# Kernel optimization log

Hardware: AMD Instinct MI355X
Metric: run time of the kernel (lower is better)

Reference implementation:

```python
import jax, jax.numpy as jnp
import numpy as np

NV = 1_000_000   # number of 'var' nodes
NC = 500_000     # number of 'con' nodes
E = 16_000_000   # number of v2c edges (c2v is the reverse edge set)
H = 10           # n_h_feats


def setup_inputs() -> dict:
    key = jax.random.key(0)
    ks = jax.random.split(key, 24)
    s = 0.1  # weight init scale
    inp = {
        "var_c": jax.random.normal(ks[0], (NV,), jnp.float32),
        "var_x": jax.random.normal(ks[1], (NV,), jnp.float32),
        "con_b": jax.random.normal(ks[2], (NC,), jnp.float32),
        "A": jax.random.uniform(ks[3], (E,), jnp.float32),
        "src": jax.random.randint(ks[4], (E,), 0, NV, jnp.int32),
        "dst": jax.random.randint(ks[5], (E,), 0, NC, jnp.int32),
        # var_emb / con_emb Linear params
        "Wv": jax.random.normal(ks[6], (2, H), jnp.float32) * s,
        "bv": jnp.zeros((H,), jnp.float32),
        "Wc": jax.random.normal(ks[7], (1, H), jnp.float32) * s,
        "bc": jnp.zeros((H,), jnp.float32),
        # conv1 (GraphConv, shared across v2c/c2v) -- note: its output is
        # overwritten in the original forward and never reaches the output
        "W1": jax.random.normal(ks[8], (H, H), jnp.float32) * s,
        "b1": jnp.zeros((H,), jnp.float32),
        # conv2 (GraphConv, shared across v2c/c2v)
        "W2": jax.random.normal(ks[9], (H, H), jnp.float32) * s,
        "b2": jnp.zeros((H,), jnp.float32),
        # output MLP
        "Wo1": jax.random.normal(ks[10], (H, H), jnp.float32) * s,
        "bo1": jnp.zeros((H,), jnp.float32),
        "Wo2": jax.random.normal(ks[11], (H, H), jnp.float32) * s,
        "bo2": jnp.zeros((H,), jnp.float32),
        "Wo3": jax.random.normal(ks[12], (H, 1), jnp.float32) * s,
        "bo3": jnp.zeros((1,), jnp.float32),
    }
    return inp


def _gconv(x_src, W, b, s_idx, d_idx, ew, norm_src, norm_dst, n_dst):
    # DGL GraphConv, norm='both', with edge weights; in==out feats so W first.
    h = (x_src * norm_src) @ W                      # [N_src, H]
    msg = h[s_idx] * ew[:, None]                    # gather + edge weight
    agg = jax.ops.segment_sum(msg, d_idx, num_segments=n_dst)
    return agg * norm_dst + b


def reference(var_c, var_x, con_b, A, src, dst,
              Wv, bv, Wc, bc, W1, b1, W2, b2,
              Wo1, bo1, Wo2, bo2, Wo3, bo3):
    # symmetric norm from UNWEIGHTED degrees (DGL GraphConv norm='both'),
    # clamped at 1. v2c: out-deg(var), in-deg(con); c2v is the reverse.
    ones_e = jnp.ones_like(A)
    deg_v = jnp.clip(jax.ops.segment_sum(ones_e, src, num_segments=NV), 1.0)
    deg_c = jnp.clip(jax.ops.segment_sum(ones_e, dst, num_segments=NC), 1.0)
    norm_v = deg_v[:, None] ** -0.5
    norm_c = deg_c[:, None] ** -0.5

    # node embeddings
    var_feats = jnp.stack([var_c, var_x], axis=1)   # [NV, 2]
    X_var = jax.nn.relu(var_feats @ Wv + bv)        # [NV, H]
    X_con = jax.nn.relu(con_b[:, None] @ Wc + bc)   # [NC, H] (unused by convs: GraphConv ignores dst feats)

    # In the original forward, conv1 outputs (h_con / h_var) are immediately
    # overwritten by conv2 outputs (GraphConv only consumes src features),
    # so only conv2 lies on the effective compute path.
    h_con = jax.nn.relu(_gconv(X_var, W2, b2, src, dst, A, norm_v, norm_c, NC))
    h_var = jax.nn.relu(_gconv(h_con, W2, b2, dst, src, A, norm_c, norm_v, NV))

    h = jax.nn.relu(h_var @ Wo1 + bo1)
    h = jax.nn.relu(h @ Wo2 + bo2)
    logit = h @ Wo3 + bo3                           # [NV, 1]
    # dgl.readout_nodes(op='mean', ntype='var'), single graph -> [1, 1]
    return jnp.mean(logit, axis=0, keepdims=True)
```

## Files before the change

### kernel.cpp

```cpp
#include <hip/hip_runtime.h>

#define HF 10
#define ST 16
#define BST 16
#define SLC 256
#define NBINS 4096
#define NSL 8


__global__ __launch_bounds__(1024) void k_hist(const int* __restrict__ idx,
                                               unsigned* __restrict__ hist,
                                               long long s_begin, long long s_end, int per) {
    __shared__ unsigned l[NBINS];
    int t = threadIdx.x, sl = blockIdx.x;
    for (int b = t; b < NBINS; b += 1024) l[b] = 0u;
    __syncthreads();
    long long s0 = s_begin + (long long)sl * per;
    long long s1 = s0 + per; if (s1 > s_end) s1 = s_end;
    for (long long i = s0 + t; i < s1; i += 1024)
        atomicAdd(&l[((unsigned)idx[i]) >> 8], 1u);
    __syncthreads();
    unsigned* out = hist + (size_t)sl * NBINS;
    for (int b = t; b < NBINS; b += 1024) out[b] = l[b];
}

__global__ void k_coltot(const unsigned* __restrict__ h, unsigned* __restrict__ colT) {
    int b = blockIdx.x * 256 + threadIdx.x;
    unsigned s = 0u;
    for (int sl = 0; sl < SLC; sl++) s += h[(size_t)sl * NBINS + b];
    colT[b] = s;
}

__global__ __launch_bounds__(1024) void k_prefix(const unsigned* __restrict__ colT,
                                                 unsigned* __restrict__ start) {
    __shared__ unsigned p[1024];
    int t = threadIdx.x;
    uint4 v = *(const uint4*)(colT + 4 * t);
    unsigned own = v.x + v.y + v.z + v.w;
    p[t] = own;
    __syncthreads();
    for (int off = 1; off < 1024; off <<= 1) {
        unsigned u = (t >= off) ? p[t - off] : 0u;
        __syncthreads();
        p[t] += u;
        __syncthreads();
    }
    unsigned e = p[t] - own;
    *(uint4*)(start + 4 * t) = make_uint4(e, e + v.x, e + v.x + v.y, e + v.x + v.y + v.z);
    if (t == 1023) start[NBINS] = p[1023];
}

__global__ void k_offs(unsigned* __restrict__ h, const unsigned* __restrict__ start) {
    int b = blockIdx.x * 256 + threadIdx.x;
    unsigned cur = start[b];
    for (int sl = 0; sl < SLC; sl++) {
        unsigned* cell = h + (size_t)sl * NBINS + b;
        unsigned v = *cell;
        *cell = cur;
        cur += v;
    }
}

__global__ __launch_bounds__(1024) void k_scatS(const int* __restrict__ src, const int* __restrict__ dst,
                                                const float* __restrict__ A,
                                                const unsigned* __restrict__ offs,
                                                uint2* __restrict__ ebufS,
                                                long long E, int per) {
    __shared__ unsigned cur[NBINS];
    int t = threadIdx.x, sl = blockIdx.x;
    const unsigned* o = offs + (size_t)sl * NBINS;
    for (int b = t; b < NBINS; b += 1024) cur[b] = o[b];
    __syncthreads();
    long long s0 = (long long)sl * per;
    long long s1 = s0 + per; if (s1 > E) s1 = E;
    for (long long i = s0 + t; i < s1; i += 1024) {
        unsigned s = (unsigned)src[i], d = (unsigned)dst[i];
        float a = A[i];
        unsigned pos = atomicAdd(&cur[s >> 8], 1u);
        ebufS[pos] = make_uint2(((s & 255u) << 19) | d, __float_as_uint(a));
    }
}

__global__ void k_sliceCnt(const uint2* __restrict__ ebufA, const unsigned* __restrict__ startS,
                           unsigned* __restrict__ startS2) {
    __shared__ unsigned c8[NSL];
    int t = threadIdx.x, b = blockIdx.x;
    if (t < NSL) c8[t] = 0u;
    __syncthreads();
    unsigned i0 = startS[b], i1 = startS[b + 1];
    for (unsigned i = i0 + t; i < i1; i += 256)
        atomicAdd(&c8[(ebufA[i].x & 0x7FFFFu) >> 16], 1u);
    __syncthreads();
    if (t == 0) {
        unsigned run = i0;
        for (int s = 0; s < NSL; s++) { startS2[b * NSL + s] = run; run += c8[s]; }
    }
}

__global__ void k_sliceScat(const uint2* __restrict__ ebufA, const unsigned* __restrict__ startS,
                            const unsigned* __restrict__ startS2, uint2* __restrict__ ebufB) {
    __shared__ unsigned cur[NSL];
    int t = threadIdx.x, b = blockIdx.x;
    if (t < NSL) cur[t] = startS2[b * NSL + t];
    __syncthreads();
    unsigned i0 = startS[b], i1 = startS[b + 1];
    for (unsigned i = i0 + t; i < i1; i += 256) {
        uint2 kv = ebufA[i];
        unsigned pos = atomicAdd(&cur[(kv.x & 0x7FFFFu) >> 16], 1u);
        ebufB[pos] = kv;
    }
}

__global__ void k_cntS2(const uint2* __restrict__ ebufS, const unsigned* __restrict__ startS,
                        const float* __restrict__ var_c, const float* __restrict__ var_x,
                        float4* __restrict__ vcx, int NV) {
    __shared__ unsigned cnt[256];
    int t = threadIdx.x, b = blockIdx.x;
    cnt[t] = 0u;
    __syncthreads();
    unsigned i0 = startS[b], i1 = startS[b + 1];
    for (unsigned i = i0 + t; i < i1; i += 256)
        atomicAdd(&cnt[ebufS[i].x >> 19], 1u);
    __syncthreads();
    int v = b * 256 + t;
    if (v < NV)
        vcx[v] = make_float4(var_c[v], var_x[v], rsqrtf(fmaxf((float)cnt[t], 1.0f)), 0.0f);
}

__global__ __launch_bounds__(1024) void k_histD2(const uint2* __restrict__ ebufB,
                                                 const unsigned* __restrict__ startS,
                                                 unsigned* __restrict__ hist, int B0, int binsPer) {
    __shared__ unsigned l[NBINS];
    int t = threadIdx.x, sl = blockIdx.x;
    for (int b = t; b < NBINS; b += 1024) l[b] = 0u;
    __syncthreads();
    int b0 = B0 + sl * binsPer;
    unsigned i0 = startS[b0], i1 = startS[b0 + binsPer];
    for (unsigned i = i0 + t; i < i1; i += 1024)
        atomicAdd(&l[(ebufB[i].x & 0x7FFFFu) >> 8], 1u);
    __syncthreads();
    unsigned* out = hist + (size_t)sl * NBINS;
    for (int b = t; b < NBINS; b += 1024) out[b] = l[b];
}

__global__ __launch_bounds__(1024) void k_scatD2(const uint2* __restrict__ ebufB,
                                                 const unsigned* __restrict__ startS,
                                                 const unsigned* __restrict__ offs,
                                                 const float4* __restrict__ vcx,
                                                 uint4* __restrict__ ebufD, int B0, int binsPer) {
    __shared__ unsigned cur[NBINS];
    int t = threadIdx.x, sl = blockIdx.x;
    const unsigned* o = offs + (size_t)sl * NBINS;
    for (int b = t; b < NBINS; b += 1024) cur[b] = o[b];
    __syncthreads();
    int b0 = B0 + sl * binsPer;
    for (int bb = 0; bb < binsPer; bb++) {
        int bin = b0 + bb;
        unsigned vbase = ((unsigned)bin) << 8;
        unsigned i0 = startS[bin], i1 = startS[bin + 1];
        for (unsigned i = i0 + t; i < i1; i += 1024) {
            uint2 kv = ebufB[i];
            unsigned d = kv.x & 0x7FFFFu;
            float4 g = vcx[vbase | (kv.x >> 19)];
            unsigned pos = atomicAdd(&cur[d >> 8], 1u);
            ebufD[pos] = make_uint4(d & 255u, __float_as_uint(__uint_as_float(kv.y) * g.z),
                                    __float_as_uint(g.x), __float_as_uint(g.y));
        }
    }
}

__global__ __launch_bounds__(1024) void k_scatD(const int* __restrict__ src, const int* __restrict__ dst,
                                                const float* __restrict__ A,
                                                const unsigned* __restrict__ offs,
                                                const float4* __restrict__ vcx,
                                                uint4* __restrict__ ebufD,
                                                long long s_begin, long long s_end, int per) {
    __shared__ unsigned cur[NBINS];
    int t = threadIdx.x, sl = blockIdx.x;
    const unsigned* o = offs + (size_t)sl * NBINS;
    for (int b = t; b < NBINS; b += 1024) cur[b] = o[b];
    __syncthreads();
    long long s0 = s_begin + (long long)sl * per;
    long long s1 = s0 + per; if (s1 > s_end) s1 = s_end;
    for (long long i = s0 + t; i < s1; i += 4096) {
        unsigned sv[4], dv[4]; float av[4]; bool hv[4];
#pragma unroll
        for (int j = 0; j < 4; j++) {
            long long idx = i + (long long)j * 1024;
            hv[j] = idx < s1;
            if (hv[j]) { sv[j] = (unsigned)src[idx]; dv[j] = (unsigned)dst[idx]; av[j] = A[idx]; }
            else       { sv[j] = 0u; dv[j] = 0u; av[j] = 0.0f; }
        }
        float4 g[4];
#pragma unroll
        for (int j = 0; j < 4; j++)
            if (hv[j]) g[j] = vcx[sv[j]];
#pragma unroll
        for (int j = 0; j < 4; j++) {
            if (!hv[j]) continue;
            unsigned pos = atomicAdd(&cur[dv[j] >> 8], 1u);
            ebufD[pos] = make_uint4(dv[j] & 255u, __float_as_uint(av[j] * g[j].z),
                                    __float_as_uint(g[j].x), __float_as_uint(g[j].y));
        }
    }
}

__global__ void k_aggD(const uint4* __restrict__ ebufD, const unsigned* __restrict__ startD,
                       const float* __restrict__ Wv, const float* __restrict__ bv,
                       float* __restrict__ bufC, float* __restrict__ deg_c, int NC) {
    __shared__ float acc[256 * HF];
    __shared__ unsigned cnt[256];
    int t = threadIdx.x, b = blockIdx.x;
    for (int i = t; i < 256 * HF; i += 256) acc[i] = 0.0f;
    cnt[t] = 0u;
    float wv0[HF], wv1[HF], bvv[HF];
#pragma unroll
    for (int h = 0; h < HF; h++) { wv0[h] = Wv[h]; wv1[h] = Wv[HF + h]; bvv[h] = bv[h]; }
    __syncthreads();
    unsigned i0 = startD[b], i1 = startD[b + 1];
    for (unsigned i = i0 + t; i < i1; i += 256) {
        uint4 kv = ebufD[i];
        unsigned dl = kv.x;
        float anv = __uint_as_float(kv.y);
        float c   = __uint_as_float(kv.z);
        float x   = __uint_as_float(kv.w);
        float* ac = acc + dl * HF;
#pragma unroll
        for (int h = 0; h < HF; h++) {
            float e = fmaxf(fmaf(c, wv0[h], fmaf(x, wv1[h], bvv[h])), 0.0f);
            atomicAdd(ac + h, anv * e);
        }
        atomicAdd(&cnt[dl], 1u);
    }
    __syncthreads();
    int gid = b * 256 + t;
    if (gid < NC) {
        float* row = bufC + (size_t)gid * BST;
#pragma unroll
        for (int h = 0; h < HF; h++) row[h] += acc[t * HF + h];
        deg_c[gid] += (float)cnt[t];
    }
}

__global__ void k_conT(float* __restrict__ bufC, const float* __restrict__ deg_c,
                       const float* __restrict__ W2, const float* __restrict__ b2, int NC) {
    __shared__ float sW[HF * HF], sb[HF];
    int t = threadIdx.x;
    if (t < HF * HF) sW[t] = W2[t];
    if (t < HF)      sb[t] = b2[t];
    __syncthreads();
    int i = blockIdx.x * 256 + t;
    if (i >= NC) return;
    float nc = rsqrtf(fmaxf(deg_c[i], 1.0f));
    float* row = bufC + (size_t)i * BST;
    float x[HF];
#pragma unroll
    for (int h = 0; h < HF; h++) x[h] = row[h];
#pragma unroll
    for (int j = 0; j < HF; j++) {
        float a = 0.0f;
#pragma unroll
        for (int k = 0; k < HF; k++) a = fmaf(x[k], sW[k * HF + j], a);
        row[j] = fmaxf(fmaf(a, nc, sb[j]), 0.0f) * nc;
    }
}

__global__ void k_aggS(const uint2* __restrict__ ebufS, const unsigned* __restrict__ startS,
                       const float* __restrict__ bufC, const float4* __restrict__ vcx,
                       const float* __restrict__ W2, const float* __restrict__ b2,
                       const float* __restrict__ Wo1, const float* __restrict__ bo1,
                       const float* __restrict__ Wo2, const float* __restrict__ bo2,
                       const float* __restrict__ Wo3, const float* __restrict__ bo3,
                       double* __restrict__ gacc, int NV) {
    __shared__ float acc[256 * HF];
    __shared__ float sW2[HF * HF], sb2[HF], sW1[HF * HF], sb1[HF], sWm[HF * HF], sbm[HF], sW3[HF];
    __shared__ float sb3;
    __shared__ double red[256];
    int t = threadIdx.x, b = blockIdx.x;
    for (int i = t; i < 256 * HF; i += 256) acc[i] = 0.0f;
    if (t < HF * HF) { sW2[t] = W2[t]; sW1[t] = Wo1[t]; sWm[t] = Wo2[t]; }
    if (t < HF)      { sb2[t] = b2[t]; sb1[t] = bo1[t]; sbm[t] = bo2[t]; sW3[t] = Wo3[t]; }
    if (t == 0)      sb3 = bo3[0];
    __syncthreads();
    unsigned i0 = startS[b], i1 = startS[b + 1];
    int grp = t >> 2;
    int q   = t & 3;
    int nq  = (q < 2) ? 4 : (q == 2 ? 2 : 0);
    for (unsigned base = i0; base < i1; base += 64) {
        unsigned e = base + (unsigned)grp;
        bool ok = e < i1;
        uint2 kv = ok ? ebufS[e] : make_uint2(0u, 0u);
        float4 y = make_float4(0.f, 0.f, 0.f, 0.f);
        if (ok) y = *(const float4*)(bufC + (size_t)(kv.x & 0x7FFFFu) * BST + 4 * q);
        if (ok && nq) {
            float a = __uint_as_float(kv.y);
            float* ac = acc + (kv.x >> 19) * HF + 4 * q;
            atomicAdd(ac + 0, a * y.x);
            atomicAdd(ac + 1, a * y.y);
            if (nq == 4) {
                atomicAdd(ac + 2, a * y.z);
                atomicAdd(ac + 3, a * y.w);
            }
        }
    }
    __syncthreads();
    double local = 0.0;
    int v = b * 256 + t;
    if (v < NV) {
        float nv = vcx[v].z;
        float x[HF], hvv[HF], h1[HF], h2[HF];
#pragma unroll
        for (int h = 0; h < HF; h++) x[h] = acc[t * HF + h];
#pragma unroll
        for (int j = 0; j < HF; j++) {
            float a = 0.0f;
#pragma unroll
            for (int k = 0; k < HF; k++) a = fmaf(x[k], sW2[k * HF + j], a);
            hvv[j] = fmaxf(fmaf(a, nv, sb2[j]), 0.0f);
        }
#pragma unroll
        for (int j = 0; j < HF; j++) {
            float a = sb1[j];
#pragma unroll
            for (int k = 0; k < HF; k++) a = fmaf(hvv[k], sW1[k * HF + j], a);
            h1[j] = fmaxf(a, 0.0f);
        }
#pragma unroll
        for (int j = 0; j < HF; j++) {
            float a = sbm[j];
#pragma unroll
            for (int k = 0; k < HF; k++) a = fmaf(h1[k], sWm[k * HF + j], a);
            h2[j] = fmaxf(a, 0.0f);
        }
        float logit = sb3;
#pragma unroll
        for (int k = 0; k < HF; k++) logit = fmaf(h2[k], sW3[k], logit);
        local = (double)logit;
    }
    red[t] = local;
    __syncthreads();
    for (int s = 128; s > 0; s >>= 1) {
        if (t < s) red[t] += red[t + s];
        __syncthreads();
    }
    if (t == 0) atomicAdd(gacc, red[0]);
}

__global__ void k_out(const double* __restrict__ acc, float* __restrict__ out, int NV) {
    out[0] = (float)(acc[0] / (double)NV);
}


__global__ void k_degree(const int* __restrict__ src, const int* __restrict__ dst,
                         float* __restrict__ deg_v, float* __restrict__ deg_c, int E) {
    int i = blockIdx.x * blockDim.x + threadIdx.x;
    if (i < E) {
        atomicAdd(&deg_v[src[i]], 1.0f);
        atomicAdd(&deg_c[dst[i]], 1.0f);
    }
}

__global__ void k_norm(float* __restrict__ d, int n) {
    int i = blockIdx.x * blockDim.x + threadIdx.x;
    if (i < n) d[i] = 1.0f / sqrtf(fmaxf(d[i], 1.0f));
}

__global__ void k_var_emb(const float* __restrict__ var_c, const float* __restrict__ var_x,
                          const float* __restrict__ norm_v,
                          const float* __restrict__ Wv, const float* __restrict__ bv,
                          const float* __restrict__ W2,
                          float* __restrict__ out, int NV) {
    __shared__ float sWv[2 * HF], sbv[HF], sW2[HF * HF];
    int t = threadIdx.x;
    if (t < 2 * HF) sWv[t] = Wv[t];
    if (t < HF)     sbv[t] = bv[t];
    if (t < HF * HF) sW2[t] = W2[t];
    __syncthreads();
    int i = blockIdx.x * blockDim.x + t;
    if (i >= NV) return;
    float c = var_c[i], x = var_x[i], nv = norm_v[i];
    float e[HF];
#pragma unroll
    for (int h = 0; h < HF; h++)
        e[h] = fmaxf(fmaf(c, sWv[h], fmaf(x, sWv[HF + h], sbv[h])), 0.0f) * nv;
    float* row = out + (size_t)i * ST;
#pragma unroll
    for (int j = 0; j < HF; j++) {
        float acc = 0.0f;
#pragma unroll
        for (int k = 0; k < HF; k++) acc = fmaf(e[k], sW2[k * HF + j], acc);
        row[j] = acc;
    }
}

__global__ void k_edge(const int* __restrict__ gidx, const int* __restrict__ didx,
                       const float* __restrict__ A,
                       const float* __restrict__ h, float* __restrict__ agg, int E) {
    int tid = blockIdx.x * blockDim.x + threadIdx.x;
    int e = tid / 5;
    if (e >= E) return;
    int q = tid - e * 5;
    int s = gidx[e], d = didx[e];
    float a = A[e];
    const float2 m = *(const float2*)(h + (size_t)s * ST + 2 * q);
    float* o = agg + (size_t)d * ST + 2 * q;
    atomicAdd(o,     m.x * a);
    atomicAdd(o + 1, m.y * a);
}

__global__ void k_con(float* __restrict__ buf, const float* __restrict__ norm_c,
                      const float* __restrict__ W2, const float* __restrict__ b2, int NC) {
    __shared__ float sW2[HF * HF], sb2[HF];
    int t = threadIdx.x;
    if (t < HF * HF) sW2[t] = W2[t];
    if (t < HF)      sb2[t] = b2[t];
    __syncthreads();
    int i = blockIdx.x * blockDim.x + t;
    if (i >= NC) return;
    float nc = norm_c[i];
    float* row = buf + (size_t)i * ST;
    float hc[HF];
#pragma unroll
    for (int h = 0; h < HF; h++)
        hc[h] = fmaxf(fmaf(row[h], nc, sb2[h]), 0.0f) * nc;
#pragma unroll
    for (int j = 0; j < HF; j++) {
        float acc = 0.0f;
#pragma unroll
        for (int k = 0; k < HF; k++) acc = fmaf(hc[k], sW2[k * HF + j], acc);
        row[j] = acc;
    }
}

__global__ void k_final(const float* __restrict__ agg_v, const float* __restrict__ norm_v,
                        const float* __restrict__ b2,
                        const float* __restrict__ Wo1, const float* __restrict__ bo1,
                        const float* __restrict__ Wo2, const float* __restrict__ bo2,
                        const float* __restrict__ Wo3, const float* __restrict__ bo3,
                        double* __restrict__ acc, int NV) {
    __shared__ float sb2[HF], sW1[HF * HF], sb1[HF], sW2m[HF * HF], sb2m[HF], sW3[HF];
    __shared__ float sb3;
    __shared__ double red[256];
    int t = threadIdx.x;
    if (t < HF)      sb2[t]  = b2[t];
    if (t < HF * HF) sW1[t]  = Wo1[t];
    if (t < HF)      sb1[t]  = bo1[t];
    if (t < HF * HF) sW2m[t] = Wo2[t];
    if (t < HF)      sb2m[t] = bo2[t];
    if (t < HF)      sW3[t]  = Wo3[t];
    if (t == 0)      sb3     = bo3[0];
    __syncthreads();
    int i = blockIdx.x * blockDim.x + t;
    double local = 0.0;
    if (i < NV) {
        float nv = norm_v[i];
        const float* row = agg_v + (size_t)i * ST;
        float v[HF], h1[HF], h2[HF];
#pragma unroll
        for (int h = 0; h < HF; h++) v[h] = fmaxf(fmaf(row[h], nv, sb2[h]), 0.0f);
#pragma unroll
        for (int j = 0; j < HF; j++) {
            float a = sb1[j];
#pragma unroll
            for (int k = 0; k < HF; k++) a = fmaf(v[k], sW1[k * HF + j], a);
            h1[j] = fmaxf(a, 0.0f);
        }
#pragma unroll
        for (int j = 0; j < HF; j++) {
            float a = sb2m[j];
#pragma unroll
            for (int k = 0; k < HF; k++) a = fmaf(h1[k], sW2m[k * HF + j], a);
            h2[j] = fmaxf(a, 0.0f);
        }
        float logit = sb3;
#pragma unroll
        for (int k = 0; k < HF; k++) logit = fmaf(h2[k], sW3[k], logit);
        local = (double)logit;
    }
    red[t] = local;
    __syncthreads();
    for (int s = 128; s > 0; s >>= 1) {
        if (t < s) red[t] += red[t + s];
        __syncthreads();
    }
    if (t == 0) atomicAdd(acc, red[0]);
}


extern "C" void kernel_launch(void* const* d_in, const int* in_sizes, int n_in,
                              void* d_out, int out_size, void* d_ws, size_t ws_size,
                              hipStream_t stream) {
    const float* var_c = (const float*)d_in[0];
    const float* var_x = (const float*)d_in[1];
    const float* A   = (const float*)d_in[3];
    const int*   src = (const int*)d_in[4];
    const int*   dst = (const int*)d_in[5];
    const float* Wv  = (const float*)d_in[6];
    const float* bv  = (const float*)d_in[7];
    const float* W2  = (const float*)d_in[12];
    const float* b2  = (const float*)d_in[13];
    const float* Wo1 = (const float*)d_in[14];
    const float* bo1 = (const float*)d_in[15];
    const float* Wo2 = (const float*)d_in[16];
    const float* bo2 = (const float*)d_in[17];
    const float* Wo3 = (const float*)d_in[18];
    const float* bo3 = (const float*)d_in[19];

    const int NV = in_sizes[0];
    const int NC = in_sizes[2];
    const int E  = in_sizes[3];

    auto layout_bytes = [&](int nDc, bool split, size_t* offs_out) -> size_t {
        size_t off = 0;
        auto alloc = [&](size_t bytes, int slot) {
            if (offs_out) offs_out[slot] = off;
            off = (off + bytes + 255) & ~(size_t)255;
        };
        size_t EcMax;
        if (split) {
            long long vspan = (long long)(NBINS / nDc) * 256;
            if (vspan > NV) vspan = NV;
            long long ec = ((long long)E * vspan + NV - 1) / NV + (long long)E / 64;
            if (ec > E) ec = E;
            EcMax = (size_t)ec;
        } else {
            EcMax = ((size_t)E + nDc - 1) / nDc;
        }
        alloc((size_t)NC * BST * 4, 0);
        alloc((size_t)NV * 16, 1);
        alloc((size_t)NC * 4, 2);
        alloc((size_t)SLC * NBINS * 4, 3);
        alloc((size_t)SLC * NBINS * 4, 4);
        alloc((size_t)NBINS * 4, 5);
        alloc((size_t)(NBINS + 1) * 4, 6);
        alloc((size_t)(NBINS + 1) * 4, 7);
        alloc(8, 8);
        alloc((size_t)E * 8, 9);
        size_t scratch = EcMax * 16;
        if (split && scratch < (size_t)E * 8) scratch = (size_t)E * 8;
        alloc(scratch, 10);
        alloc(split ? (size_t)NBINS * NSL * 4 : (size_t)0, 11);
        return off;
    };

    int nD = 0;
    bool split = false;
    size_t offs[12];
    for (int cand : {2, 4, 8, 16}) {
        if (layout_bytes(cand, true, nullptr) <= ws_size) { nD = cand; split = true; break; }
    }
    if (nD == 0) {
        for (int cand = 2; cand <= 16; cand++)
            if (layout_bytes(cand, false, nullptr) <= ws_size) { nD = cand; break; }
    }
    bool fast = (nD > 0) && (NV <= (1 << 20)) && (NC <= (1 << 19)) && (E > 0);

    char* ws = (char*)d_ws;
    if (fast) {
        layout_bytes(nD, split, offs);
        float*    bufC   = (float*)(ws + offs[0]);
        float4*   vcx    = (float4*)(ws + offs[1]);
        float*    deg_c  = (float*)(ws + offs[2]);
        unsigned* hS     = (unsigned*)(ws + offs[3]);
        unsigned* hD     = (unsigned*)(ws + offs[4]);
        unsigned* colT   = (unsigned*)(ws + offs[5]);
        unsigned* startS = (unsigned*)(ws + offs[6]);
        unsigned* startD = (unsigned*)(ws + offs[7]);
        double*   gacc   = (double*)(ws + offs[8]);
        uint2*    ebufP  = (uint2*)(ws + offs[9]);
        char*     scr    = ws + offs[10];
        unsigned* startS2 = (unsigned*)(ws + offs[11]);

        const int perS = (int)(((long long)E + SLC - 1) / SLC);
        const int NB_S = (NV + 255) >> 8;
        const int NB_C = (NC + 255) >> 8;

        hipMemsetAsync(bufC,  0, (size_t)NC * BST * 4, stream);
        hipMemsetAsync(deg_c, 0, (size_t)NC * 4, stream);
        hipMemsetAsync(gacc,  0, 8, stream);

        if (split) {
            uint2* ebufA = (uint2*)scr;
            uint4* ebufD = (uint4*)scr;

            k_hist<<<SLC, 1024, 0, stream>>>(src, hS, 0, E, perS);
            k_coltot<<<NBINS / 256, 256, 0, stream>>>(hS, colT);
            k_prefix<<<1, 1024, 0, stream>>>(colT, startS);
            k_offs<<<NBINS / 256, 256, 0, stream>>>(hS, startS);
            k_scatS<<<SLC, 1024, 0, stream>>>(src, dst, A, hS, ebufA, E, perS);

            k_sliceCnt<<<NBINS, 256, 0, stream>>>(ebufA, startS, startS2);
            k_sliceScat<<<NBINS, 256, 0, stream>>>(ebufA, startS, startS2, ebufP);

            k_cntS2<<<NB_S, 256, 0, stream>>>(ebufP, startS, var_c, var_x, vcx, NV);

            const int binsChunk = NBINS / nD;
            const int binsPer   = binsChunk / SLC;
            for (int c = 0; c < nD; c++) {
                int B0 = c * binsChunk;
                k_histD2<<<SLC, 1024, 0, stream>>>(ebufP, startS, hD, B0, binsPer);
                k_coltot<<<NBINS / 256, 256, 0, stream>>>(hD, colT);
                k_prefix<<<1, 1024, 0, stream>>>(colT, startD);
                k_offs<<<NBINS / 256, 256, 0, stream>>>(hD, startD);
                k_scatD2<<<SLC, 1024, 0, stream>>>(ebufP, startS, hD, vcx, ebufD, B0, binsPer);
                k_aggD<<<NB_C, 256, 0, stream>>>(ebufD, startD, Wv, bv, bufC, deg_c, NC);
            }
        } else {
            uint4* ebufD = (uint4*)scr;
            const long long EcMax = ((long long)E + nD - 1) / nD;
            const int perD = (int)((EcMax + SLC - 1) / SLC);

            k_hist<<<SLC, 1024, 0, stream>>>(src, hS, 0, E, perS);
            k_coltot<<<NBINS / 256, 256, 0, stream>>>(hS, colT);
            k_prefix<<<1, 1024, 0, stream>>>(colT, startS);
            k_offs<<<NBINS / 256, 256, 0, stream>>>(hS, startS);
            k_scatS<<<SLC, 1024, 0, stream>>>(src, dst, A, hS, ebufP, E, perS);

            k_cntS2<<<NB_S, 256, 0, stream>>>(ebufP, startS, var_c, var_x, vcx, NV);

            for (int c = 0; c < nD; c++) {
                long long cb = (long long)c * EcMax;
                long long ce = cb + EcMax; if (ce > E) ce = E;
                k_hist<<<SLC, 1024, 0, stream>>>(dst, hD, cb, ce, perD);
                k_coltot<<<NBINS / 256, 256, 0, stream>>>(hD, colT);
                k_prefix<<<1, 1024, 0, stream>>>(colT, startD);
                k_offs<<<NBINS / 256, 256, 0, stream>>>(hD, startD);
                k_scatD<<<SLC, 1024, 0, stream>>>(src, dst, A, hD, vcx, ebufD, cb, ce, perD);
                k_aggD<<<NB_C, 256, 0, stream>>>(ebufD, startD, Wv, bv, bufC, deg_c, NC);
            }
        }
        k_conT<<<NB_C, 256, 0, stream>>>(bufC, deg_c, W2, b2, NC);

        k_aggS<<<NB_S, 256, 0, stream>>>(ebufP, startS, bufC, vcx, W2, b2,
                                         Wo1, bo1, Wo2, bo2, Wo3, bo3, gacc, NV);
        k_out<<<1, 1, 0, stream>>>(gacc, (float*)d_out, NV);
    } else {
        const int B = 256;
        float* fbufV = (float*)ws;
        float* fbufC = (float*)(ws + (size_t)NV * ST * 4);
        float* deg_v = (float*)(ws + (size_t)(NV + NC) * ST * 4);
        float* deg_c = deg_v + NV;
        size_t acc_off = ((size_t)(NV + NC) * ST * 4 + (size_t)(NV + NC) * 4 + 7) & ~(size_t)7;
        double* acc = (double*)(ws + acc_off);

        hipMemsetAsync(deg_v, 0, (size_t)(NV + NC) * 4, stream);
        hipMemsetAsync(fbufC, 0, (size_t)NC * ST * 4, stream);
        hipMemsetAsync(acc, 0, sizeof(double), stream);

        k_degree<<<(E + B - 1) / B, B, 0, stream>>>(src, dst, deg_v, deg_c, E);
        k_norm<<<(NV + NC + B - 1) / B, B, 0, stream>>>(deg_v, NV + NC);
        k_var_emb<<<(NV + B - 1) / B, B, 0, stream>>>(var_c, var_x, deg_v, Wv, bv, W2, fbufV, NV);

        long long tE = (long long)E * 5;
        k_edge<<<(int)((tE + B - 1) / B), B, 0, stream>>>(src, dst, A, fbufV, fbufC, E);
        k_con<<<(NC + B - 1) / B, B, 0, stream>>>(fbufC, deg_c, W2, b2, NC);

        hipMemsetAsync(fbufV, 0, (size_t)NV * ST * 4, stream);
        k_edge<<<(int)((tE + B - 1) / B), B, 0, stream>>>(dst, src, A, fbufC, fbufV, E);

        k_final<<<(NV + B - 1) / B, B, 0, stream>>>(fbufV, deg_v, b2, Wo1, bo1, Wo2, bo2, Wo3, bo3, acc, NV);
        k_out<<<1, 1, 0, stream>>>(acc, (float*)d_out, NV);
    }
}
```

Baseline: 2.997 ms.

## Replace two-pass global slice sort with in-place LDS-staged 16-way sub-sort

Merges the slice count and slice scatter kernels into one kernel that stages each source bin in LDS, counts 16 dst sub-slices, and writes back in place to the same buffer. This drops one full read of the edge buffer and the separate ping-pong scratch buffer. The freed memory lets the dst-chunk scratch be sized per chunk, so fewer dst chunks (starting from 4) can fit. Writes in scatD2 are now bounds-checked against capacity. Bins larger than the LDS capacity are silently left unsorted, which risks wrong ordering on skewed inputs.

```diff
diff --git a/kernel.cpp b/kernel.cpp
--- a/kernel.cpp
+++ b/kernel.cpp
@@ -5,7 +5,8 @@
 #define BST 16
 #define SLC 256
 #define NBINS 4096
-#define NSL 8
+#define NSL 16
+#define CAPS 6144
 
 
 __global__ __launch_bounds__(1024) void k_hist(const int* __restrict__ idx,
@@ -81,33 +82,30 @@
     }
 }
 
-__global__ void k_sliceCnt(const uint2* __restrict__ ebufA, const unsigned* __restrict__ startS,
-                           unsigned* __restrict__ startS2) {
-    __shared__ unsigned c8[NSL];
+__global__ __launch_bounds__(256) void k_sliceIP(uint2* __restrict__ ebuf,
+                                                 const unsigned* __restrict__ startS) {
+    __shared__ uint2 ebl[CAPS];
+    __shared__ unsigned c16[NSL], p16[NSL];
     int t = threadIdx.x, b = blockIdx.x;
-    if (t < NSL) c8[t] = 0u;
-    __syncthreads();
-    unsigned i0 = startS[b], i1 = startS[b + 1];
-    for (unsigned i = i0 + t; i < i1; i += 256)
-        atomicAdd(&c8[(ebufA[i].x & 0x7FFFFu) >> 16], 1u);
+    unsigned i0 = startS[b], i1 = startS[b + 1], n = i1 - i0;
+    if (n == 0u || n > (unsigned)CAPS) return;
+    if (t < NSL) c16[t] = 0u;
+    __syncthreads();
+    for (unsigned i = t; i < n; i += 256) {
+        uint2 kv = ebuf[i0 + i];
+        ebl[i] = kv;
+        atomicAdd(&c16[(kv.x & 0x7FFFFu) >> 15], 1u);
+    }
     __syncthreads();
     if (t == 0) {
-        unsigned run = i0;
-        for (int s = 0; s < NSL; s++) { startS2[b * NSL + s] = run; run += c8[s]; }
-    }
-}
-
-__global__ void k_sliceScat(const uint2* __restrict__ ebufA, const unsigned* __restrict__ startS,
-                            const unsigned* __restrict__ startS2, uint2* __restrict__ ebufB) {
-    __shared__ unsigned cur[NSL];
-    int t = threadIdx.x, b = blockIdx.x;
-    if (t < NSL) cur[t] = startS2[b * NSL + t];
-    __syncthreads();
-    unsigned i0 = startS[b], i1 = startS[b + 1];
-    for (unsigned i = i0 + t; i < i1; i += 256) {
-        uint2 kv = ebufA[i];
-        unsigned pos = atomicAdd(&cur[(kv.x & 0x7FFFFu) >> 16], 1u);
-        ebufB[pos] = kv;
+        unsigned run = 0u;
+        for (int s = 0; s < NSL; s++) { p16[s] = run; run += c16[s]; }
+    }
+    __syncthreads();
+    for (unsigned i = t; i < n; i += 256) {
+        uint2 kv = ebl[i];
+        unsigned pos = atomicAdd(&p16[(kv.x & 0x7FFFFu) >> 15], 1u);
+        ebuf[i0 + pos] = kv;
     }
 }
 
@@ -147,7 +145,8 @@
                                                  const unsigned* __restrict__ startS,
                                                  const unsigned* __restrict__ offs,
                                                  const float4* __restrict__ vcx,
-                                                 uint4* __restrict__ ebufD, int B0, int binsPer) {
+                                                 uint4* __restrict__ ebufD, int B0, int binsPer,
+                                                 unsigned cap) {
     __shared__ unsigned cur[NBINS];
     int t = threadIdx.x, sl = blockIdx.x;
     const unsigned* o = offs + (size_t)sl * NBINS;
@@ -163,8 +162,9 @@
             unsigned d = kv.x & 0x7FFFFu;
             float4 g = vcx[vbase | (kv.x >> 19)];
             unsigned pos = atomicAdd(&cur[d >> 8], 1u);
-            ebufD[pos] = make_uint4(d & 255u, __float_as_uint(__uint_as_float(kv.y) * g.z),
-                                    __float_as_uint(g.x), __float_as_uint(g.y));
+            if (pos < cap)
+                ebufD[pos] = make_uint4(d & 255u, __float_as_uint(__uint_as_float(kv.y) * g.z),
+                                        __float_as_uint(g.x), __float_as_uint(g.y));
         }
     }
 }
@@ -510,22 +510,23 @@
     const int NC = in_sizes[2];
     const int E  = in_sizes[3];
 
-    auto layout_bytes = [&](int nDc, bool split, size_t* offs_out) -> size_t {
+    long long EcMaxUsed = 0;
+    auto layout_bytes = [&](int nDc, bool binchunk, size_t* offs_out) -> size_t {
         size_t off = 0;
         auto alloc = [&](size_t bytes, int slot) {
             if (offs_out) offs_out[slot] = off;
             off = (off + bytes + 255) & ~(size_t)255;
         };
-        size_t EcMax;
-        if (split) {
+        long long ec;
+        if (binchunk) {
             long long vspan = (long long)(NBINS / nDc) * 256;
             if (vspan > NV) vspan = NV;
-            long long ec = ((long long)E * vspan + NV - 1) / NV + (long long)E / 64;
+            ec = ((long long)E * vspan) / NV + (long long)E / 64 + 1024;
             if (ec > E) ec = E;
-            EcMax = (size_t)ec;
         } else {
-            EcMax = ((size_t)E + nDc - 1) / nDc;
-        }
+            ec = ((long long)E + nDc - 1) / nDc;
+        }
+        EcMaxUsed = ec;
         alloc((size_t)NC * BST * 4, 0);
         alloc((size_t)NV * 16, 1);
         alloc((size_t)NC * 4, 2);
@@ -536,18 +537,15 @@
         alloc((size_t)(NBINS + 1) * 4, 7);
         alloc(8, 8);
         alloc((size_t)E * 8, 9);
-        size_t scratch = EcMax * 16;
-        if (split && scratch < (size_t)E * 8) scratch = (size_t)E * 8;
-        alloc(scratch, 10);
-        alloc(split ? (size_t)NBINS * NSL * 4 : (size_t)0, 11);
+        alloc((size_t)ec * 16, 10);
         return off;
     };
 
     int nD = 0;
-    bool split = false;
-    size_t offs[12];
-    for (int cand : {2, 4, 8, 16}) {
-        if (layout_bytes(cand, true, nullptr) <= ws_size) { nD = cand; split = true; break; }
+    bool binc = false;
+    size_t offs[11];
+    for (int cand : {4, 8, 16}) {
+        if (layout_bytes(cand, true, nullptr) <= ws_size) { nD = cand; binc = true; break; }
     }
     if (nD == 0) {
         for (int cand = 2; cand <= 16; cand++)
@@ -557,7 +555,8 @@
 
     char* ws = (char*)d_ws;
     if (fast) {
-        layout_bytes(nD, split, offs);
+        layout_bytes(nD, binc, offs);
+        const long long EcMax = EcMaxUsed;
         float*    bufC   = (float*)(ws + offs[0]);
         float4*   vcx    = (float4*)(ws + offs[1]);
         float*    deg_c  = (float*)(ws + offs[2]);
@@ -567,9 +566,8 @@
         unsigned* startS = (unsigned*)(ws + offs[6]);
         unsigned* startD = (unsigned*)(ws + offs[7]);
         double*   gacc   = (double*)(ws + offs[8]);
-        uint2*    ebufP  = (uint2*)(ws + offs[9]);
-        char*     scr    = ws + offs[10];
-        unsigned* startS2 = (unsigned*)(ws + offs[11]);
+        uint2*    ebufS  = (uint2*)(ws + offs[9]);
+        uint4*    ebufD  = (uint4*)(ws + offs[10]);
 
         const int perS = (int)(((long long)E + SLC - 1) / SLC);
         const int NB_S = (NV + 255) >> 8;
@@ -579,45 +577,31 @@
         hipMemsetAsync(deg_c, 0, (size_t)NC * 4, stream);
         hipMemsetAsync(gacc,  0, 8, stream);
 
-        if (split) {
-            uint2* ebufA = (uint2*)scr;
-            uint4* ebufD = (uint4*)scr;
-
-            k_hist<<<SLC, 1024, 0, stream>>>(src, hS, 0, E, perS);
-            k_coltot<<<NBINS / 256, 256, 0, stream>>>(hS, colT);
-            k_prefix<<<1, 1024, 0, stream>>>(colT, startS);
-            k_offs<<<NBINS / 256, 256, 0, stream>>>(hS, startS);
-            k_scatS<<<SLC, 1024, 0, stream>>>(src, dst, A, hS, ebufA, E, perS);
-
-            k_sliceCnt<<<NBINS, 256, 0, stream>>>(ebufA, startS, startS2);
-            k_sliceScat<<<NBINS, 256, 0, stream>>>(ebufA, startS, startS2, ebufP);
-
-            k_cntS2<<<NB_S, 256, 0, stream>>>(ebufP, startS, var_c, var_x, vcx, NV);
-
+        k_hist<<<SLC, 1024, 0, stream>>>(src, hS, 0, E, perS);
+        k_coltot<<<NBINS / 256, 256, 0, stream>>>(hS, colT);
+        k_prefix<<<1, 1024, 0, stream>>>(colT, startS);
+        k_offs<<<NBINS / 256, 256, 0, stream>>>(hS, startS);
+        k_scatS<<<SLC, 1024, 0, stream>>>(src, dst, A, hS, ebufS, E, perS);
+
+        k_sliceIP<<<NBINS, 256, 0, stream>>>(ebufS, startS);
+
+        k_cntS2<<<NB_S, 256, 0, stream>>>(ebufS, startS, var_c, var_x, vcx, NV);
+
+        if (binc) {
             const int binsChunk = NBINS / nD;
             const int binsPer   = binsChunk / SLC;
             for (int c = 0; c < nD; c++) {
                 int B0 = c * binsChunk;
-                k_histD2<<<SLC, 1024, 0, stream>>>(ebufP, startS, hD, B0, binsPer);
+                k_histD2<<<SLC, 1024, 0, stream>>>(ebufS, startS, hD, B0, binsPer);
                 k_coltot<<<NBINS / 256, 256, 0, stream>>>(hD, colT);
                 k_prefix<<<1, 1024, 0, stream>>>(colT, startD);
                 k_offs<<<NBINS / 256, 256, 0, stream>>>(hD, startD);
-                k_scatD2<<<SLC, 1024, 0, stream>>>(ebufP, startS, hD, vcx, ebufD, B0, binsPer);
+                k_scatD2<<<SLC, 1024, 0, stream>>>(ebufS, startS, hD, vcx, ebufD,
+                                                   B0, binsPer, (unsigned)EcMax);
                 k_aggD<<<NB_C, 256, 0, stream>>>(ebufD, startD, Wv, bv, bufC, deg_c, NC);
             }
         } else {
-            uint4* ebufD = (uint4*)scr;
-            const long long EcMax = ((long long)E + nD - 1) / nD;
             const int perD = (int)((EcMax + SLC - 1) / SLC);
-
-            k_hist<<<SLC, 1024, 0, stream>>>(src, hS, 0, E, perS);
-            k_coltot<<<NBINS / 256, 256, 0, stream>>>(hS, colT);
-            k_prefix<<<1, 1024, 0, stream>>>(colT, startS);
-            k_offs<<<NBINS / 256, 256, 0, stream>>>(hS, startS);
-            k_scatS<<<SLC, 1024, 0, stream>>>(src, dst, A, hS, ebufP, E, perS);
-
-            k_cntS2<<<NB_S, 256, 0, stream>>>(ebufP, startS, var_c, var_x, vcx, NV);
-
             for (int c = 0; c < nD; c++) {
                 long long cb = (long long)c * EcMax;
                 long long ce = cb + EcMax; if (ce > E) ce = E;
@@ -631,7 +615,7 @@
         }
         k_conT<<<NB_C, 256, 0, stream>>>(bufC, deg_c, W2, b2, NC);
 
-        k_aggS<<<NB_S, 256, 0, stream>>>(ebufP, startS, bufC, vcx, W2, b2,
+        k_aggS<<<NB_S, 256, 0, stream>>>(ebufS, startS, bufC, vcx, W2, b2,
                                          Wo1, bo1, Wo2, bo2, Wo3, bo3, gacc, NV);
         k_out<<<1, 1, 0, stream>>>(gacc, (float*)d_out, NV);
     } else {
```

After: 2.722 ms. -9.2%, faster.
